# Kernel tuning notes

Hardware: AMD Instinct MI355X
Metric: run time of the kernel (lower is better)

The kernel has to match this reference:

```python
import jax, jax.numpy as jnp
import numpy as np


def _pad_kernel_like(kernel_oc0, H, W, ks):
    # torch: F.pad(k,(p,p,p,p)) then if shape mismatch F.pad(k,(0,1,0,1))
    p = (H - ks) // 2
    extra = H - (ks + 2 * p)  # 0 or 1
    return jnp.pad(kernel_oc0, ((0, 0), (p, p + extra), (p, p + extra)))


def setup_inputs() -> dict:
    key = jax.random.key(0)
    k1, k2 = jax.random.split(key)
    B, C, H, W = 8, 16, 128, 128
    O, KS = 32, 9
    x = jax.random.normal(k1, (B, C, H, W), dtype=jnp.float32)
    # kaiming_uniform-ish init scale
    fan_in = C * KS * KS
    bound = float(np.sqrt(6.0 / fan_in))
    kernel = jax.random.uniform(k2, (O, C, KS, KS), dtype=jnp.float32,
                                minval=-bound, maxval=bound)
    return {"x": x, "kernel": kernel}


def reference(x, kernel):
    # x: [B,C,H,W] float32, kernel: [O,C,ks,ks] float32
    B, C, H, W = x.shape
    O, ks = kernel.shape[0], kernel.shape[-1]
    # Faithful to original bug: only kernel[:, 0] is used for every input channel.
    k = _pad_kernel_like(kernel[:, 0], H, W, ks)  # [O,H,W]
    # 4f optical FFT convolution: ifftshift -> FFT -> multiply -> IFFT -> fftshift -> |.|
    Fx = jnp.fft.fft2(jnp.fft.ifftshift(x, axes=(-2, -1)))   # [B,C,H,W] complex64
    Fk = jnp.fft.fft2(jnp.fft.ifftshift(k, axes=(-2, -1)))   # [O,H,W]   complex64
    prod = Fx[:, None, :, :, :] * Fk[None, :, None, :, :]    # [B,O,C,H,W]
    field = jnp.fft.fftshift(jnp.fft.ifft2(prod), axes=(-2, -1))
    out_pc = jnp.abs(field)                                  # per-(out,in)-channel intensity
    return out_pc.sum(axis=2)                                # [B,O,H,W]
```

## Files before the change

### kernel.cpp

```cpp
#include <hip/hip_runtime.h>


typedef __attribute__((ext_vector_type(8)))  short  short8;
typedef __attribute__((ext_vector_type(16))) float  float16v;
typedef __attribute__((ext_vector_type(4)))  float  float4v;
typedef __attribute__((ext_vector_type(4)))  unsigned int uint4v;

#define XR_ROWS 138
#define XR_RDW  72
#define XR_CH_DW (XR_ROWS * XR_RDW)
#define XR_CH_B  (XR_CH_DW * 4)
#define BPRE_OFF ((size_t)128 * XR_ROWS * 288)
#define CHB 3168

__device__ __forceinline__ unsigned int f2bf(float f) {
    union { float f; unsigned int u; } a; a.f = f;
    unsigned int u = a.u;
    u += 0x7fffu + ((u >> 16) & 1u);
    return u >> 16;
}

#if __has_builtin(__builtin_amdgcn_alignbit)
#define ALIGN16(hi_, lo_) __builtin_amdgcn_alignbit((hi_), (lo_), 16)
#else
#define ALIGN16(hi_, lo_) \
    (unsigned int)((((unsigned long long)(hi_) << 32) | (lo_)) >> 16)
#endif

#define FRAG_EVEN(q_) __builtin_bit_cast(short8, (uint4v){                    \
        wnd[(q_)+0], wnd[(q_)+1], wnd[(q_)+2], wnd[(q_)+3]})
#define FRAG_ODD(q_)  __builtin_bit_cast(short8, (uint4v){                    \
        ALIGN16(wnd[(q_)+1], wnd[(q_)+0]),                                    \
        ALIGN16(wnd[(q_)+2], wnd[(q_)+1]),                                    \
        ALIGN16(wnd[(q_)+3], wnd[(q_)+2]),                                    \
        ALIGN16(wnd[(q_)+4], wnd[(q_)+3])})

__device__ __forceinline__ void gload_lds16(const void* g, void* l) {
    __builtin_amdgcn_global_load_lds(
        (const __attribute__((address_space(1))) unsigned int*)g,
        (__attribute__((address_space(3))) unsigned int*)l, 16, 0, 0);
}

__global__ __launch_bounds__(256)
void optical_prep_69698729279498(const float* __restrict__ x,
                                 const float* __restrict__ kern,
                                 unsigned int* __restrict__ xr,
                                 uint4v* __restrict__ bpre) {
    const int t = blockIdx.x * 256 + threadIdx.x;
    const int bc = blockIdx.y;
    const int rem = t - 9984;
    if (t < XR_CH_DW) {
        int r   = t / 72;
        int ccd = t - r * 72;
        int cc  = 2 * ccd;
        const float* xp = x + (bc << 14) + ((r & 127) << 7);
        float v0 = xp[(132 - cc) & 127];
        float v1 = xp[(131 - cc) & 127];
        xr[(size_t)bc * XR_CH_DW + t] = f2bf(v0) | (f2bf(v1) << 16);
    } else if (bc == 0 && rem >= 0 && rem < 64) {
        const int l  = rem;
        const int o  = l & 31;
        const int hi = l >> 5;
        for (int ti = 0; ti < 9; ++ti) {
            unsigned int pk[4];
#pragma unroll
            for (int ee = 0; ee < 4; ++ee) {
                int tj_a = 8 * hi + 2 * ee, tj_b = tj_a + 1;
                float va = (tj_a <= 8) ? kern[o * 1296 + ti * 9 + tj_a] : 0.f;
                float vb = (tj_b <= 8) ? kern[o * 1296 + ti * 9 + tj_b] : 0.f;
                pk[ee] = f2bf(va) | (f2bf(vb) << 16);
            }
            bpre[ti * 64 + l] = (uint4v){pk[0], pk[1], pk[2], pk[3]};
        }
    }
}

__global__ __launch_bounds__(256, 2)
void optical_conv_69698729279498(const unsigned int* __restrict__ xr,
                                 const uint4v* __restrict__ bpre,
                                 float* __restrict__ out) {
    __shared__ __align__(16) unsigned short ldsb[16 * (CHB / 2)];

    const int tid = threadIdx.x;
    const int l   = tid & 63;
    const int w   = tid >> 6;
    const int ph  = w & 1;
    const int cg  = w >> 1;
    const int i0  = blockIdx.x * 2;
    const int b   = blockIdx.y;

    const int jm  = l & 15;
    const int rl  = (l >> 4) & 1;
    const int hi  = l >> 5;

    const int wstart = (i0 >= 4) ? (i0 - 4) : (i0 + 124);
    const char* xr8 = (const char*)xr;
#pragma unroll
    for (int cw = 0; cw < 4; ++cw) {
        const int ch = 4 * w + cw;
        const char* src = xr8 + ((size_t)((b * 16 + ch) * XR_ROWS + wstart)) * 288;
        char* dst = (char*)ldsb + ch * CHB;
        gload_lds16(src + 0 * 1024 + l * 16, dst + 0 * 1024);
        gload_lds16(src + 1 * 1024 + l * 16, dst + 1 * 1024);
        gload_lds16(src + 2 * 1024 + l * 16, dst + 2 * 1024);
        if (l < 6)
            gload_lds16(src + 3072 + l * 16, dst + 3072);
    }

    short8 Bf[9];
#pragma unroll
    for (int ti = 0; ti < 9; ++ti)
        Bf[ti] = __builtin_bit_cast(short8, bpre[ti * 64 + l]);

    __syncthreads();

    float16v acc[4];
#pragma unroll
    for (int pp = 0; pp < 4; ++pp)
#pragma unroll
        for (int e = 0; e < 16; ++e) acc[pp][e] = 0.f;
    float16v zero16;
#pragma unroll
    for (int e = 0; e < 16; ++e) zero16[e] = 0.f;

    const char* lb = (const char*)ldsb
                   + (240 - 16 * jm + 16 * hi) + (1 + rl) * 288
                   + cg * 8 * CHB;

    for (int c = 0; c < 8; ++c) {
        float16v D[4];
#pragma unroll
        for (int ti = 0; ti < 9; ++ti) {
            const char* p = lb + (8 - ti) * 288;
            uint4v w0 = *(const uint4v*)p;
            uint4v w1 = *(const uint4v*)(p + 16);
            unsigned int wnd[8] = {w0.x, w0.y, w0.z, w0.w,
                                   w1.x, w1.y, w1.z, w1.w};
            short8 f0, f1, f2, f3;
            if (ph == 0) {
                f0 = FRAG_ODD(3);  f1 = FRAG_EVEN(3);
                f2 = FRAG_ODD(2);  f3 = FRAG_EVEN(2);
            } else {
                f0 = FRAG_ODD(1);  f1 = FRAG_EVEN(1);
                f2 = FRAG_ODD(0);  f3 = FRAG_EVEN(0);
            }
            D[0] = __builtin_amdgcn_mfma_f32_32x32x16_bf16(f0, Bf[ti], ti ? D[0] : zero16, 0, 0, 0);
            D[1] = __builtin_amdgcn_mfma_f32_32x32x16_bf16(f1, Bf[ti], ti ? D[1] : zero16, 0, 0, 0);
            D[2] = __builtin_amdgcn_mfma_f32_32x32x16_bf16(f2, Bf[ti], ti ? D[2] : zero16, 0, 0, 0);
            D[3] = __builtin_amdgcn_mfma_f32_32x32x16_bf16(f3, Bf[ti], ti ? D[3] : zero16, 0, 0, 0);
        }
#pragma unroll
        for (int pp = 0; pp < 4; ++pp)
#pragma unroll
            for (int e = 0; e < 16; ++e) acc[pp][e] += fabsf(D[pp][e]);
        lb += CHB;
    }

    __syncthreads();
    float* otile = (float*)ldsb;
    const int obase_l = (l & 31) * 129 + 32 * (l >> 5) + 4 * ph;
    if (cg == 1) {
#pragma unroll
        for (int pp = 0; pp < 4; ++pp)
#pragma unroll
            for (int reg = 0; reg < 16; ++reg)
                otile[obase_l + (reg >> 3) * 4128 + 8 * (reg & 3)
                      + 64 * ((reg >> 2) & 1) + pp] = acc[pp][reg];
    }
    __syncthreads();
    if (cg == 0) {
#pragma unroll
        for (int pp = 0; pp < 4; ++pp)
#pragma unroll
            for (int reg = 0; reg < 16; ++reg) {
                const int idx = obase_l + (reg >> 3) * 4128 + 8 * (reg & 3)
                              + 64 * ((reg >> 2) & 1) + pp;
                otile[idx] += acc[pp][reg];
            }
    }
    __syncthreads();

    {
        const int pair = tid >> 2;
        const int q    = tid & 3;
        const int r    = pair >> 5;
        const int o    = pair & 31;
        const float* src = otile + pair * 129 + q * 32;
        float* dstg = out + ((((size_t)(b * 32 + o)) * 128 + (i0 + r)) << 7) + q * 32;
#pragma unroll
        for (int k4 = 0; k4 < 8; ++k4) {
            float4v v = (float4v){src[4 * k4], src[4 * k4 + 1],
                                  src[4 * k4 + 2], src[4 * k4 + 3]};
            *(float4v*)&dstg[4 * k4] = v;
        }
    }
}

extern "C" void kernel_launch(void* const* d_in, const int* in_sizes, int n_in,
                              void* d_out, int out_size, void* d_ws, size_t ws_size,
                              hipStream_t stream) {
    const float* x = (const float*)d_in[0];
    const float* kern = (const float*)d_in[1];
    float* out = (float*)d_out;
    unsigned int* xr = (unsigned int*)d_ws;
    uint4v* bpre = (uint4v*)((char*)d_ws + BPRE_OFF);

    hipLaunchKernelGGL(optical_prep_69698729279498, dim3(40, 128),
                       dim3(256), 0, stream, x, kern, xr, bpre);
    hipLaunchKernelGGL(optical_conv_69698729279498, dim3(64, 8), dim3(256),
                       0, stream, xr, bpre, out);
}
```

Measured before the change: 94.45 us.

## Fuse bf16 prep into conv kernel, loading and converting x directly into LDS

Drops the separate prep kernel that wrote a bf16, shifted and padded copy of x and the packed kernel weights to workspace. The conv kernel now gathers fp32 x straight from global memory, converts it to bf16 and writes it into LDS, and builds the B fragments from the raw kernel weights itself. This removes one launch and the round trip through workspace. In exchange, each block re-reads 11 rows per channel in fp32 (the halo rows are read by several blocks), and the scattered scalar loads and large register arrays may cost latency and occupancy.

```diff
diff --git a/kernel.cpp b/kernel.cpp
--- a/kernel.cpp
+++ b/kernel.cpp
@@ -6,12 +6,11 @@
 typedef __attribute__((ext_vector_type(4)))  float  float4v;
 typedef __attribute__((ext_vector_type(4)))  unsigned int uint4v;
 
-#define XR_ROWS 138
-#define XR_RDW  72
-#define XR_CH_DW (XR_ROWS * XR_RDW)
-#define XR_CH_B  (XR_CH_DW * 4)
-#define BPRE_OFF ((size_t)128 * XR_ROWS * 288)
-#define CHB 3168
+#define NROW 11
+#define NCC  144
+#define CHSZ (NROW * NCC)
+#define CHB  3168
+#define NSLOT (16 * NROW * 72)
 
 __device__ __forceinline__ unsigned int f2bf(float f) {
     union { float f; unsigned int u; } a; a.f = f;
@@ -35,51 +34,25 @@
         ALIGN16(wnd[(q_)+3], wnd[(q_)+2]),                                    \
         ALIGN16(wnd[(q_)+4], wnd[(q_)+3])})
 
-__device__ __forceinline__ void gload_lds16(const void* g, void* l) {
-    __builtin_amdgcn_global_load_lds(
-        (const __attribute__((address_space(1))) unsigned int*)g,
-        (__attribute__((address_space(3))) unsigned int*)l, 16, 0, 0);
-}
-
-__global__ __launch_bounds__(256)
-void optical_prep_69698729279498(const float* __restrict__ x,
+#define LOAD_SLOT(s_, v0_, v1_, ad_)                                         \
+    {                                                                        \
+        int ch  = (s_) / 792;                                                \
+        int rem = (s_) - 792 * ch;                                           \
+        int rr  = rem / 72;                                                  \
+        int ccd = rem - 72 * rr;                                             \
+        int cc  = 2 * ccd;                                                   \
+        int xrow = (i0 - 4 + rr) & 127;                                      \
+        const float* xp = xb + (ch << 14) + (xrow << 7);                     \
+        v0_ = xp[(132 - cc) & 127];                                          \
+        v1_ = xp[(131 - cc) & 127];                                          \
+        ad_ = ch * CHSZ + rr * NCC + cc;                                     \
+    }
+
+__global__ __launch_bounds__(256, 2)
+void optical_conv_69698729279498(const float* __restrict__ x,
                                  const float* __restrict__ kern,
-                                 unsigned int* __restrict__ xr,
-                                 uint4v* __restrict__ bpre) {
-    const int t = blockIdx.x * 256 + threadIdx.x;
-    const int bc = blockIdx.y;
-    const int rem = t - 9984;
-    if (t < XR_CH_DW) {
-        int r   = t / 72;
-        int ccd = t - r * 72;
-        int cc  = 2 * ccd;
-        const float* xp = x + (bc << 14) + ((r & 127) << 7);
-        float v0 = xp[(132 - cc) & 127];
-        float v1 = xp[(131 - cc) & 127];
-        xr[(size_t)bc * XR_CH_DW + t] = f2bf(v0) | (f2bf(v1) << 16);
-    } else if (bc == 0 && rem >= 0 && rem < 64) {
-        const int l  = rem;
-        const int o  = l & 31;
-        const int hi = l >> 5;
-        for (int ti = 0; ti < 9; ++ti) {
-            unsigned int pk[4];
-#pragma unroll
-            for (int ee = 0; ee < 4; ++ee) {
-                int tj_a = 8 * hi + 2 * ee, tj_b = tj_a + 1;
-                float va = (tj_a <= 8) ? kern[o * 1296 + ti * 9 + tj_a] : 0.f;
-                float vb = (tj_b <= 8) ? kern[o * 1296 + ti * 9 + tj_b] : 0.f;
-                pk[ee] = f2bf(va) | (f2bf(vb) << 16);
-            }
-            bpre[ti * 64 + l] = (uint4v){pk[0], pk[1], pk[2], pk[3]};
-        }
-    }
-}
-
-__global__ __launch_bounds__(256, 2)
-void optical_conv_69698729279498(const unsigned int* __restrict__ xr,
-                                 const uint4v* __restrict__ bpre,
                                  float* __restrict__ out) {
-    __shared__ __align__(16) unsigned short ldsb[16 * (CHB / 2)];
+    __shared__ __align__(16) unsigned short ldsb[16 * CHSZ];
 
     const int tid = threadIdx.x;
     const int l   = tid & 63;
@@ -93,24 +66,49 @@
     const int rl  = (l >> 4) & 1;
     const int hi  = l >> 5;
 
-    const int wstart = (i0 >= 4) ? (i0 - 4) : (i0 + 124);
-    const char* xr8 = (const char*)xr;
-#pragma unroll
-    for (int cw = 0; cw < 4; ++cw) {
-        const int ch = 4 * w + cw;
-        const char* src = xr8 + ((size_t)((b * 16 + ch) * XR_ROWS + wstart)) * 288;
-        char* dst = (char*)ldsb + ch * CHB;
-        gload_lds16(src + 0 * 1024 + l * 16, dst + 0 * 1024);
-        gload_lds16(src + 1 * 1024 + l * 16, dst + 1 * 1024);
-        gload_lds16(src + 2 * 1024 + l * 16, dst + 2 * 1024);
-        if (l < 6)
-            gload_lds16(src + 3072 + l * 16, dst + 3072);
+    const float* xb = x + ((size_t)b << 18);
+
+    {
+        float v0a[25], v1a[25]; int aa[25];
+#pragma unroll
+        for (int k = 0; k < 25; ++k) {
+            int s = tid + 256 * k;
+            LOAD_SLOT(s, v0a[k], v1a[k], aa[k]);
+        }
+#pragma unroll
+        for (int k = 0; k < 25; ++k) {
+            unsigned int pk2 = f2bf(v0a[k]) | (f2bf(v1a[k]) << 16);
+            *(unsigned int*)&ldsb[aa[k]] = pk2;
+        }
+#pragma unroll
+        for (int k = 0; k < 25; ++k) {
+            int s = tid + 256 * (25 + k);
+            if (s > NSLOT - 1) s = NSLOT - 1;
+            LOAD_SLOT(s, v0a[k], v1a[k], aa[k]);
+        }
+#pragma unroll
+        for (int k = 0; k < 25; ++k) {
+            unsigned int pk2 = f2bf(v0a[k]) | (f2bf(v1a[k]) << 16);
+            *(unsigned int*)&ldsb[aa[k]] = pk2;
+        }
     }
 
     short8 Bf[9];
-#pragma unroll
-    for (int ti = 0; ti < 9; ++ti)
-        Bf[ti] = __builtin_bit_cast(short8, bpre[ti * 64 + l]);
+    {
+        const int o = l & 31;
+#pragma unroll
+        for (int ti = 0; ti < 9; ++ti) {
+            unsigned int pk[4];
+#pragma unroll
+            for (int ee = 0; ee < 4; ++ee) {
+                int tj_a = 8 * hi + 2 * ee, tj_b = tj_a + 1;
+                float va = (tj_a <= 8) ? kern[o * 1296 + ti * 9 + tj_a] : 0.f;
+                float vb = (tj_b <= 8) ? kern[o * 1296 + ti * 9 + tj_b] : 0.f;
+                pk[ee] = f2bf(va) | (f2bf(vb) << 16);
+            }
+            Bf[ti] = __builtin_bit_cast(short8, (uint4v){pk[0], pk[1], pk[2], pk[3]});
+        }
+    }
 
     __syncthreads();
 
@@ -202,11 +200,6 @@
     const float* x = (const float*)d_in[0];
     const float* kern = (const float*)d_in[1];
     float* out = (float*)d_out;
-    unsigned int* xr = (unsigned int*)d_ws;
-    uint4v* bpre = (uint4v*)((char*)d_ws + BPRE_OFF);
-
-    hipLaunchKernelGGL(optical_prep_69698729279498, dim3(40, 128),
-                       dim3(256), 0, stream, x, kern, xr, bpre);
     hipLaunchKernelGGL(optical_conv_69698729279498, dim3(64, 8), dim3(256),
-                       0, stream, xr, bpre, out);
+                       0, stream, x, kern, out);
 }
```

Result: slower. 97.99 us (+3.8%).
